# Performance work log

Measured on AMD Instinct MI355X. Metric: run time of the kernel, lower is better.

## Reference

```python
import jax, jax.numpy as jnp
import numpy as np

B, S, D_MODEL, D_KEY = 4, 2048, 1024, 128


def setup_inputs() -> dict:
    key = jax.random.key(0)
    kq, kk, kv, kwq, kwk, kwv = jax.random.split(key, 6)
    queries = jax.random.normal(kq, (B, S, D_MODEL), dtype=jnp.float32)
    keys = jax.random.normal(kk, (B, S, D_MODEL), dtype=jnp.float32)
    values = jax.random.normal(kv, (B, S, D_MODEL), dtype=jnp.float32)
    # causal mask: 1 where attention is allowed (j <= i), 0 otherwise
    mask = jnp.broadcast_to(jnp.tril(jnp.ones((S, S), dtype=jnp.int32)), (B, S, S))
    # torch nn.Linear weights are [out, in]; init ~ U(-1/sqrt(in), 1/sqrt(in))
    bound = 1.0 / np.sqrt(D_MODEL)
    Wq = jax.random.uniform(kwq, (D_KEY, D_MODEL), jnp.float32, -bound, bound)
    Wk = jax.random.uniform(kwk, (D_KEY, D_MODEL), jnp.float32, -bound, bound)
    Wv = jax.random.uniform(kwv, (D_KEY, D_MODEL), jnp.float32, -bound, bound)
    return {"queries": queries, "keys": keys, "values": values, "mask": mask,
            "Wq": Wq, "Wk": Wk, "Wv": Wv}


def reference(queries, keys, values, mask, Wq, Wk, Wv):
    d_key = Wq.shape[0]
    q = jnp.einsum('bsd,kd->bsk', queries, Wq)   # [B,S,d_key]
    k = jnp.einsum('bsd,kd->bsk', keys, Wk)
    v = jnp.einsum('bsd,kd->bsk', values, Wv)
    attn = jnp.einsum('bqk,bsk->bqs', q, k) / jnp.sqrt(jnp.float32(d_key))  # [B,S,S]
    attn = jnp.where(mask == 0, -jnp.inf, attn)
    attn = jax.nn.softmax(attn, axis=-1)
    return jnp.einsum('bqs,bsk->bqk', attn, v)   # [B,S,d_key]
```

## Files before the change

kernel.cpp:

```cpp
#include <hip/hip_runtime.h>
#include <hip/hip_bf16.h>

#define NB 4
#define SEQ 2048
#define DMODEL 1024
#define DKEY 128

using f32x4  = __attribute__((ext_vector_type(4))) float;
using bf16x8 = __attribute__((ext_vector_type(8))) short;
using u16x4  = __attribute__((ext_vector_type(4))) unsigned short;
using u16x8  = __attribute__((ext_vector_type(8))) unsigned short;

__device__ __forceinline__ unsigned short f2bf(float f) {
  __hip_bfloat16 h = __float2bfloat16(f);
  return __builtin_bit_cast(unsigned short, h);
}
__device__ __forceinline__ void gload16(const void* g, void* l) {
  __builtin_amdgcn_global_load_lds(
      (const __attribute__((address_space(1))) void*)g,
      (__attribute__((address_space(3))) void*)l, 16, 0, 0);
}

__global__ __launch_bounds__(256) void wconv_kernel(
    const float* __restrict__ Wq, const float* __restrict__ Wk,
    const float* __restrict__ Wv, unsigned short* __restrict__ Wb)
{
  int id = blockIdx.x * 256 + threadIdx.x;
  const float* src = (id < 16384) ? Wq : (id < 32768) ? Wk : Wv;
  int off = (id & 16383) * 8;
  float4 a = *reinterpret_cast<const float4*>(&src[off]);
  float4 b = *reinterpret_cast<const float4*>(&src[off + 4]);
  u16x8 p = { f2bf(a.x), f2bf(a.y), f2bf(a.z), f2bf(a.w),
              f2bf(b.x), f2bf(b.y), f2bf(b.z), f2bf(b.w) };
  *reinterpret_cast<u16x8*>(&Wb[(size_t)(id >> 14) * 131072 + off]) = p;
}

__global__ __launch_bounds__(256, 2) void proj_kernel(
    const float* __restrict__ Xq, const float* __restrict__ Xk, const float* __restrict__ Xv,
    const unsigned short* __restrict__ Wb,
    unsigned short* __restrict__ Yq, unsigned short* __restrict__ Yk,
    unsigned short* __restrict__ Vt)
{
  const int z = blockIdx.z;
  const float* X = (z == 0) ? Xq : (z == 1) ? Xk : Xv;
  const unsigned short* W = Wb + (size_t)z * 131072;

  __shared__ alignas(16) unsigned short XL[64 * 512];
  __shared__ alignas(16) unsigned short WL[2][128 * 32];

  const int t     = threadIdx.x;
  const int lane  = t & 63;
  const int w     = t >> 6;
  const int lr    = lane & 15;
  const int hi    = lane >> 4;
  const int rbase = hi * 4;
  const long m0   = (long)blockIdx.x * 64;
  const int arow  = w * 16 + lr;

  const int wg_row[2] = { (0 * 256 + t) >> 2, (1 * 256 + t) >> 2 };
  const int wg_col[2] = { ((((0 * 256 + t) & 3) ^ (wg_row[0] & 3)) << 3),
                          ((((1 * 256 + t) & 3) ^ (wg_row[1] & 3)) << 3) };

#define W_ISSUE(ks) do {                                                      \
    const int _s = (ks) & 1;                                                  \
    _Pragma("unroll")                                                         \
    for (int i = 0; i < 2; ++i)                                               \
      gload16(&W[(size_t)wg_row[i] * DMODEL + (ks) * 32 + wg_col[i]],         \
              &WL[_s][(i * 256 + w * 64) * 8]);                               \
  } while (0)

#define P1_LOAD(cbase) do {                                                   \
    for (int jb = 0; jb < 8; ++jb) {                                          \
      float4 v[4];                                                            \
      _Pragma("unroll")                                                       \
      for (int u = 0; u < 4; ++u) {                                           \
        int f = (jb * 4 + u) * 256 + t;                                       \
        int row = f >> 7, c4 = (f & 127) << 2;                                \
        v[u] = *reinterpret_cast<const float4*>(                              \
            &X[(m0 + row) * (long)DMODEL + (cbase) + c4]);                    \
      }                                                                       \
      _Pragma("unroll")                                                       \
      for (int u = 0; u < 4; ++u) {                                           \
        int f = (jb * 4 + u) * 256 + t;                                       \
        int row = f >> 7, c4 = (f & 127) << 2;                                \
        u16x4 p = { f2bf(v[u].x), f2bf(v[u].y), f2bf(v[u].z), f2bf(v[u].w) }; \
        *reinterpret_cast<u16x4*>(                                            \
            &XL[row * 512 + (((c4 >> 3) ^ (row & 7)) << 3)                    \
                + ((c4 >> 2) & 1) * 4]) = p;                                  \
      }                                                                       \
    }                                                                         \
  } while (0)

#define PJ_STEP(gks) do {                                                     \
    if ((gks) < 31) asm volatile("s_waitcnt vmcnt(2)" ::: "memory");          \
    else            asm volatile("s_waitcnt vmcnt(0)" ::: "memory");          \
    __builtin_amdgcn_s_barrier();                                             \
    {                                                                         \
      const int _s  = (gks) & 1;                                              \
      const int _gr = ((gks) & 15) * 4 + hi;                                  \
      bf16x8 a = *reinterpret_cast<const bf16x8*>(                            \
          &XL[arow * 512 + ((_gr ^ (lr & 7)) << 3)]);                         \
      _Pragma("unroll")                                                       \
      for (int n = 0; n < 8; ++n) {                                           \
        const int wrow = n * 16 + lr;                                         \
        bf16x8 b = *reinterpret_cast<const bf16x8*>(                          \
            &WL[_s][wrow * 32 + ((hi ^ (wrow & 3)) << 3)]);                   \
        acc[n] = __builtin_amdgcn_mfma_f32_16x16x32_bf16(a, b, acc[n], 0, 0, 0); \
      }                                                                       \
    }                                                                         \
    __builtin_amdgcn_s_barrier();                                             \
    if ((gks) + 2 < 32) W_ISSUE((gks) + 2);                                   \
  } while (0)

  f32x4 acc[8];
  const f32x4 zero = {0.f, 0.f, 0.f, 0.f};
#pragma unroll
  for (int n = 0; n < 8; ++n) acc[n] = zero;

  P1_LOAD(0);
  __syncthreads();
  W_ISSUE(0);
  W_ISSUE(1);
  for (int ks = 0; ks < 16; ++ks) PJ_STEP(ks);

  P1_LOAD(512);
  __syncthreads();
  for (int ks = 16; ks < 32; ++ks) PJ_STEP(ks);

#undef W_ISSUE
#undef P1_LOAD
#undef PJ_STEP

  if (z != 2) {
    unsigned short* Y = (z == 0) ? Yq : Yk;
#pragma unroll
    for (int n = 0; n < 8; ++n)
#pragma unroll
      for (int r = 0; r < 4; ++r) {
        long row = m0 + w * 16 + rbase + r;
        Y[row * DKEY + n * 16 + lr] = f2bf(acc[n][r]);
      }
  } else {
    unsigned short* Tl = XL;
    __syncthreads();
#pragma unroll
    for (int n = 0; n < 8; ++n)
#pragma unroll
      for (int r = 0; r < 4; ++r)
        Tl[(n * 16 + lr) * 72 + (w * 16 + rbase + r)] = f2bf(acc[n][r]);
    __syncthreads();
    const int bb = (int)(m0 >> 11);
    const int s0 = (int)(m0 & 2047);
#pragma unroll
    for (int i = 0; i < 4; ++i) {
      int id = t + 256 * i;
      int dr = id >> 3;
      int c8 = (id & 7) << 3;
      u16x8 v = *reinterpret_cast<const u16x8*>(&Tl[dr * 72 + c8]);
      *reinterpret_cast<u16x8*>(&Vt[((size_t)bb * DKEY + dr) * SEQ + s0 + c8]) = v;
    }
  }
}

__global__ __launch_bounds__(512, 2) void attn_kernel(
    const unsigned short* __restrict__ Q,
    const unsigned short* __restrict__ K,
    const unsigned short* __restrict__ Vt,
    float* __restrict__ O)
{
  const int  L    = blockIdx.x;
  const int  b    = (L & 7) >> 1;
  const int  qt   = 63 - (((L >> 3) << 1) | (L & 1));
  const int  q0   = qt * 32;
  const long base = (long)b * SEQ;
  const int  nt   = (q0 >> 6) + 1;
  const int  nsteps = (nt + 3) >> 2;

  __shared__ alignas(16) unsigned short Kl[4][64][128];
  __shared__ alignas(16) unsigned short Vl[4][128][64];
  __shared__ alignas(16) unsigned short Plds[8][16][72];
  __shared__ float Sm[4][32], Sl[4][32];

  const int t     = threadIdx.x;
  const int lane  = t & 63;
  const int w     = t >> 6;
  const int g     = w >> 1;
  const int wq    = w & 1;
  const int lr    = lane & 15;
  const int hi    = lane >> 4;
  const int lk    = hi * 8;
  const int rbase = hi * 4;

  bf16x8 qa[4];
  {
    const long qrow = (base + q0 + wq * 16 + lr) * (long)DKEY;
#pragma unroll
    for (int dk = 0; dk < 4; ++dk)
      qa[dk] = *reinterpret_cast<const bf16x8*>(&Q[qrow + dk * 32 + lk]);
  }

  const f32x4 zero = {0.f, 0.f, 0.f, 0.f};
  f32x4 oacc[8];
#pragma unroll
  for (int n = 0; n < 8; ++n) oacc[n] = zero;
  float m_run[4], l_run[4];
#pragma unroll
  for (int r = 0; r < 4; ++r) { m_run[r] = -1e30f; l_run[r] = 0.0f; }

  const float sc = 0.08838834764831845f;
  const unsigned short* VtB = Vt + (size_t)b * DKEY * SEQ;

  for (int st = 0; st < nsteps; ++st) {
    const int kt  = st * 4 + g;
    const bool act = kt < nt;
    const int kv0 = kt * 64;

    if (act) {
      const unsigned short* Kp = K + (base + kv0) * (long)DKEY;
#pragma unroll
      for (int it = 0; it < 8; ++it) {
        int c = it * 128 + wq * 64 + lane;
        int row = c >> 4, sl = (c & 15) ^ (row & 7);
        *reinterpret_cast<u16x8*>(&Kl[g][row][sl * 8]) =
            *reinterpret_cast<const u16x8*>(&Kp[(size_t)c * 8]);
      }
#pragma unroll
      for (int it = 0; it < 8; ++it) {
        int c = it * 128 + wq * 64 + lane;
        int d = c >> 3, sl = c & 7, slp = sl ^ (d & 7);
        *reinterpret_cast<u16x8*>(&Vl[g][d][slp * 8]) =
            *reinterpret_cast<const u16x8*>(&VtB[(size_t)d * SEQ + kv0 + sl * 8]);
      }
    }
    __syncthreads();

    if (act) {
      f32x4 s[4];
#pragma unroll
      for (int kc = 0; kc < 4; ++kc) {
        s[kc] = zero;
#pragma unroll
        for (int dk = 0; dk < 4; ++dk) {
          bf16x8 kb = *reinterpret_cast<const bf16x8*>(
              &Kl[g][kc * 16 + lr][((dk * 4 + hi) ^ (lr & 7)) * 8]);
          s[kc] = __builtin_amdgcn_mfma_f32_16x16x32_bf16(qa[dk], kb, s[kc], 0, 0, 0);
        }
      }

      const bool dmask = (kt == nt - 1);
      float x[4][4];
#pragma unroll
      for (int kc = 0; kc < 4; ++kc)
#pragma unroll
        for (int r = 0; r < 4; ++r) {
          float xv = s[kc][r] * sc;
          if (dmask) {
            int col  = kv0 + kc * 16 + lr;
            int rowq = q0 + wq * 16 + rbase + r;
            if (col > rowq) xv = -1e30f;
          }
          x[kc][r] = xv;
        }

#pragma unroll
      for (int r = 0; r < 4; ++r) {
        float tm = fmaxf(fmaxf(x[0][r], x[1][r]), fmaxf(x[2][r], x[3][r]));
        tm = fmaxf(tm, __shfl_xor(tm, 1));
        tm = fmaxf(tm, __shfl_xor(tm, 2));
        tm = fmaxf(tm, __shfl_xor(tm, 4));
        tm = fmaxf(tm, __shfl_xor(tm, 8));
        float mnew = fmaxf(m_run[r], tm);
        float scl  = __expf(m_run[r] - mnew);
        m_run[r] = mnew;
        float ps = 0.0f;
#pragma unroll
        for (int kc = 0; kc < 4; ++kc) {
          float pp = __expf(x[kc][r] - mnew);
          ps += pp;
          Plds[w][rbase + r][kc * 16 + lr] = f2bf(pp);
        }
        ps += __shfl_xor(ps, 1);
        ps += __shfl_xor(ps, 2);
        ps += __shfl_xor(ps, 4);
        ps += __shfl_xor(ps, 8);
        l_run[r] = l_run[r] * scl + ps;
#pragma unroll
        for (int n = 0; n < 8; ++n) oacc[n][r] *= scl;
      }

#pragma unroll
      for (int kk = 0; kk < 2; ++kk) {
        bf16x8 pa = *reinterpret_cast<const bf16x8*>(&Plds[w][lr][kk * 32 + lk]);
#pragma unroll
        for (int n = 0; n < 8; ++n) {
          bf16x8 vb = *reinterpret_cast<const bf16x8*>(
              &Vl[g][n * 16 + lr][((kk * 4 + hi) ^ (lr & 7)) * 8]);
          oacc[n] = __builtin_amdgcn_mfma_f32_16x16x32_bf16(pa, vb, oacc[n], 0, 0, 0);
        }
      }
    }
    __syncthreads();
  }

  float* Om = reinterpret_cast<float*>(&Kl[0][0][0]);
#pragma unroll
  for (int n = 0; n < 8; ++n)
#pragma unroll
    for (int r = 0; r < 4; ++r)
      Om[(g * 32 + wq * 16 + rbase + r) * 128 + n * 16 + lr] = oacc[n][r];
  if (lr == 0) {
#pragma unroll
    for (int r = 0; r < 4; ++r) {
      Sm[g][wq * 16 + rbase + r] = m_run[r];
      Sl[g][wq * 16 + rbase + r] = l_run[r];
    }
  }
  __syncthreads();

  const int row = t >> 4;
  const int c0  = (t & 15) * 8;
  float mM = fmaxf(fmaxf(Sm[0][row], Sm[1][row]), fmaxf(Sm[2][row], Sm[3][row]));
  float wts[4], lsum = 0.0f;
#pragma unroll
  for (int gv = 0; gv < 4; ++gv) {
    wts[gv] = __expf(Sm[gv][row] - mM);
    lsum += wts[gv] * Sl[gv][row];
  }
  const float linv = 1.0f / lsum;
  f32x4 o0 = zero, o1 = zero;
#pragma unroll
  for (int gv = 0; gv < 4; ++gv) {
    const float* src = &Om[(gv * 32 + row) * 128 + c0];
    f32x4 a0 = *reinterpret_cast<const f32x4*>(src);
    f32x4 a1 = *reinterpret_cast<const f32x4*>(src + 4);
    const float wt = wts[gv];
#pragma unroll
    for (int j = 0; j < 4; ++j) { o0[j] += wt * a0[j]; o1[j] += wt * a1[j]; }
  }
#pragma unroll
  for (int j = 0; j < 4; ++j) { o0[j] *= linv; o1[j] *= linv; }
  float* op = &O[(base + q0 + row) * (long)DKEY + c0];
  *reinterpret_cast<f32x4*>(op)     = o0;
  *reinterpret_cast<f32x4*>(op + 4) = o1;
}

extern "C" void kernel_launch(void* const* d_in, const int* in_sizes, int n_in,
                              void* d_out, int out_size, void* d_ws, size_t ws_size,
                              hipStream_t stream) {
  const float* Xq = (const float*)d_in[0];
  const float* Xk = (const float*)d_in[1];
  const float* Xv = (const float*)d_in[2];
  const float* Wq = (const float*)d_in[4];
  const float* Wk = (const float*)d_in[5];
  const float* Wv = (const float*)d_in[6];

  unsigned short* qp  = (unsigned short*)d_ws;
  unsigned short* kp  = qp + (size_t)NB * SEQ * DKEY;
  unsigned short* vtp = kp + (size_t)NB * SEQ * DKEY;
  unsigned short* wbp = (unsigned short*)d_out;

  hipLaunchKernelGGL(wconv_kernel, dim3(192), dim3(256), 0, stream,
                     Wq, Wk, Wv, wbp);
  dim3 g1(SEQ * NB / 64, 1, 3);
  hipLaunchKernelGGL(proj_kernel, g1, dim3(256), 0, stream,
                     Xq, Xk, Xv, wbp, qp, kp, vtp);
  hipLaunchKernelGGL(attn_kernel, dim3(256), dim3(512), 0, stream,
                     qp, kp, vtp, (float*)d_out);
}
```

Before: 70.76 us.

## Fuse weight conversion, projections and attention into one persistent kernel with flags

Merges the three launches into one kernel of 256 blocks. Each block first projects its Q, K or V tiles, converting fp32 weights to bf16 on the fly in LDS instead of in a separate pass, then sets a completion flag. The block then spin-waits on the flags for the K/V tiles it needs before running causal attention. This removes two kernel launches and the weight conversion pass, and lets projection overlap with attention. In exchange it relies on all 256 blocks being co-resident so the spin-waits cannot deadlock, adds a memset and atomics, and halves projection occupancy per block.

Result: slower. 135.6 us (+91.7%).

```diff
diff --git a/kernel.cpp b/kernel.cpp
--- a/kernel.cpp
+++ b/kernel.cpp
@@ -15,78 +15,74 @@
   __hip_bfloat16 h = __float2bfloat16(f);
   return __builtin_bit_cast(unsigned short, h);
 }
+__device__ __forceinline__ bf16x8 pack8(f32x4 lo, f32x4 hi) {
+  u16x8 p = { f2bf(lo[0]), f2bf(lo[1]), f2bf(lo[2]), f2bf(lo[3]),
+              f2bf(hi[0]), f2bf(hi[1]), f2bf(hi[2]), f2bf(hi[3]) };
+  return __builtin_bit_cast(bf16x8, p);
+}
 __device__ __forceinline__ void gload16(const void* g, void* l) {
   __builtin_amdgcn_global_load_lds(
       (const __attribute__((address_space(1))) void*)g,
       (__attribute__((address_space(3))) void*)l, 16, 0, 0);
 }
-
-__global__ __launch_bounds__(256) void wconv_kernel(
-    const float* __restrict__ Wq, const float* __restrict__ Wk,
-    const float* __restrict__ Wv, unsigned short* __restrict__ Wb)
+__device__ __forceinline__ void spinflag(int* f) {
+  while (atomicAdd(f, 0) == 0) __builtin_amdgcn_s_sleep(8);
+}
+
+#define SMEM_BYTES 150528
+
+__device__ __forceinline__ void proj_unit(
+    const float* __restrict__ X, const float* __restrict__ W,
+    unsigned short* Y, unsigned short* VtB_or_null,
+    int u, char* SMEM, int t, int* flags, int fidx)
 {
-  int id = blockIdx.x * 256 + threadIdx.x;
-  const float* src = (id < 16384) ? Wq : (id < 32768) ? Wk : Wv;
-  int off = (id & 16383) * 8;
-  float4 a = *reinterpret_cast<const float4*>(&src[off]);
-  float4 b = *reinterpret_cast<const float4*>(&src[off + 4]);
-  u16x8 p = { f2bf(a.x), f2bf(a.y), f2bf(a.z), f2bf(a.w),
-              f2bf(b.x), f2bf(b.y), f2bf(b.z), f2bf(b.w) };
-  *reinterpret_cast<u16x8*>(&Wb[(size_t)(id >> 14) * 131072 + off]) = p;
-}
-
-__global__ __launch_bounds__(256, 2) void proj_kernel(
-    const float* __restrict__ Xq, const float* __restrict__ Xk, const float* __restrict__ Xv,
-    const unsigned short* __restrict__ Wb,
-    unsigned short* __restrict__ Yq, unsigned short* __restrict__ Yk,
-    unsigned short* __restrict__ Vt)
-{
-  const int z = blockIdx.z;
-  const float* X = (z == 0) ? Xq : (z == 1) ? Xk : Xv;
-  const unsigned short* W = Wb + (size_t)z * 131072;
-
-  __shared__ alignas(16) unsigned short XL[64 * 512];
-  __shared__ alignas(16) unsigned short WL[2][128 * 32];
-
-  const int t     = threadIdx.x;
+  unsigned short* XL = reinterpret_cast<unsigned short*>(SMEM);
+  float*          WL = reinterpret_cast<float*>(SMEM + 65536);
+
   const int lane  = t & 63;
   const int w     = t >> 6;
+  const int wm    = w >> 1;
+  const int wn    = w & 1;
   const int lr    = lane & 15;
   const int hi    = lane >> 4;
   const int rbase = hi * 4;
-  const long m0   = (long)blockIdx.x * 64;
-  const int arow  = w * 16 + lr;
-
-  const int wg_row[2] = { (0 * 256 + t) >> 2, (1 * 256 + t) >> 2 };
-  const int wg_col[2] = { ((((0 * 256 + t) & 3) ^ (wg_row[0] & 3)) << 3),
-                          ((((1 * 256 + t) & 3) ^ (wg_row[1] & 3)) << 3) };
+  const long m0   = (long)u * 64;
+  const int arow  = wm * 16 + lr;
+
+  int wrow_[2], wcol_[2];
+#pragma unroll
+  for (int i = 0; i < 2; ++i) {
+    int G = i * 512 + t;
+    wrow_[i] = G >> 3;
+    wcol_[i] = (((G & 7) ^ (wrow_[i] & 7)) << 2);
+  }
 
 #define W_ISSUE(ks) do {                                                      \
-    const int _s = (ks) & 1;                                                  \
+    float* _dst = WL + ((ks) & 1) * 4096;                                     \
     _Pragma("unroll")                                                         \
     for (int i = 0; i < 2; ++i)                                               \
-      gload16(&W[(size_t)wg_row[i] * DMODEL + (ks) * 32 + wg_col[i]],         \
-              &WL[_s][(i * 256 + w * 64) * 8]);                               \
+      gload16(&W[(size_t)wrow_[i] * DMODEL + (ks) * 32 + wcol_[i]],           \
+              _dst + (i * 512 + w * 64) * 4);                                 \
   } while (0)
 
 #define P1_LOAD(cbase) do {                                                   \
-    for (int jb = 0; jb < 8; ++jb) {                                          \
+    for (int jb = 0; jb < 4; ++jb) {                                          \
       float4 v[4];                                                            \
       _Pragma("unroll")                                                       \
-      for (int u = 0; u < 4; ++u) {                                           \
-        int f = (jb * 4 + u) * 256 + t;                                       \
+      for (int u4 = 0; u4 < 4; ++u4) {                                        \
+        int f = (jb * 4 + u4) * 512 + t;                                      \
         int row = f >> 7, c4 = (f & 127) << 2;                                \
-        v[u] = *reinterpret_cast<const float4*>(                              \
+        v[u4] = *reinterpret_cast<const float4*>(                             \
             &X[(m0 + row) * (long)DMODEL + (cbase) + c4]);                    \
       }                                                                       \
       _Pragma("unroll")                                                       \
-      for (int u = 0; u < 4; ++u) {                                           \
-        int f = (jb * 4 + u) * 256 + t;                                       \
+      for (int u4 = 0; u4 < 4; ++u4) {                                        \
+        int f = (jb * 4 + u4) * 512 + t;                                      \
         int row = f >> 7, c4 = (f & 127) << 2;                                \
-        u16x4 p = { f2bf(v[u].x), f2bf(v[u].y), f2bf(v[u].z), f2bf(v[u].w) }; \
+        u16x4 p = { f2bf(v[u4].x), f2bf(v[u4].y), f2bf(v[u4].z), f2bf(v[u4].w) }; \
         *reinterpret_cast<u16x4*>(                                            \
-            &XL[row * 512 + (((c4 >> 3) ^ (row & 7)) << 3)                    \
-                + ((c4 >> 2) & 1) * 4]) = p;                                  \
+            &XL[row * 512 + ((((c4 >> 3) ^ (row & 7)) << 3)                   \
+                + ((c4 >> 2) & 1) * 4)]) = p;                                 \
       }                                                                       \
     }                                                                         \
   } while (0)
@@ -96,33 +92,36 @@
     else            asm volatile("s_waitcnt vmcnt(0)" ::: "memory");          \
     __builtin_amdgcn_s_barrier();                                             \
     {                                                                         \
-      const int _s  = (gks) & 1;                                              \
+      const float* wbase = WL + ((gks) & 1) * 4096;                           \
       const int _gr = ((gks) & 15) * 4 + hi;                                  \
       bf16x8 a = *reinterpret_cast<const bf16x8*>(                            \
           &XL[arow * 512 + ((_gr ^ (lr & 7)) << 3)]);                         \
       _Pragma("unroll")                                                       \
-      for (int n = 0; n < 8; ++n) {                                           \
-        const int wrow = n * 16 + lr;                                         \
-        bf16x8 b = *reinterpret_cast<const bf16x8*>(                          \
-            &WL[_s][wrow * 32 + ((hi ^ (wrow & 3)) << 3)]);                   \
-        acc[n] = __builtin_amdgcn_mfma_f32_16x16x32_bf16(a, b, acc[n], 0, 0, 0); \
+      for (int n = 0; n < 4; ++n) {                                           \
+        const int wrow = wn * 64 + n * 16 + lr;                               \
+        f32x4 blo = *reinterpret_cast<const f32x4*>(                          \
+            &wbase[wrow * 32 + ((((hi * 2)     ^ (wrow & 7))) << 2)]);        \
+        f32x4 bhi = *reinterpret_cast<const f32x4*>(                          \
+            &wbase[wrow * 32 + ((((hi * 2 + 1) ^ (wrow & 7))) << 2)]);        \
+        acc[n] = __builtin_amdgcn_mfma_f32_16x16x32_bf16(a, pack8(blo, bhi),  \
+                                                         acc[n], 0, 0, 0);    \
       }                                                                       \
     }                                                                         \
     __builtin_amdgcn_s_barrier();                                             \
     if ((gks) + 2 < 32) W_ISSUE((gks) + 2);                                   \
   } while (0)
 
-  f32x4 acc[8];
+  f32x4 acc[4];
   const f32x4 zero = {0.f, 0.f, 0.f, 0.f};
 #pragma unroll
-  for (int n = 0; n < 8; ++n) acc[n] = zero;
-
+  for (int n = 0; n < 4; ++n) acc[n] = zero;
+
+  __syncthreads();
   P1_LOAD(0);
   __syncthreads();
   W_ISSUE(0);
   W_ISSUE(1);
   for (int ks = 0; ks < 16; ++ks) PJ_STEP(ks);
-
   P1_LOAD(512);
   __syncthreads();
   for (int ks = 16; ks < 32; ++ks) PJ_STEP(ks);
@@ -131,57 +130,83 @@
 #undef P1_LOAD
 #undef PJ_STEP
 
-  if (z != 2) {
-    unsigned short* Y = (z == 0) ? Yq : Yk;
-#pragma unroll
-    for (int n = 0; n < 8; ++n)
+  if (Y != nullptr) {
+#pragma unroll
+    for (int n = 0; n < 4; ++n)
 #pragma unroll
       for (int r = 0; r < 4; ++r) {
-        long row = m0 + w * 16 + rbase + r;
-        Y[row * DKEY + n * 16 + lr] = f2bf(acc[n][r]);
+        long row = m0 + wm * 16 + rbase + r;
+        Y[row * DKEY + wn * 64 + n * 16 + lr] = f2bf(acc[n][r]);
       }
   } else {
-    unsigned short* Tl = XL;
+    unsigned short* Tl = reinterpret_cast<unsigned short*>(SMEM);
     __syncthreads();
 #pragma unroll
-    for (int n = 0; n < 8; ++n)
+    for (int n = 0; n < 4; ++n)
 #pragma unroll
       for (int r = 0; r < 4; ++r)
-        Tl[(n * 16 + lr) * 72 + (w * 16 + rbase + r)] = f2bf(acc[n][r]);
+        Tl[(wn * 64 + n * 16 + lr) * 72 + (wm * 16 + rbase + r)] = f2bf(acc[n][r]);
     __syncthreads();
-    const int bb = (int)(m0 >> 11);
-    const int s0 = (int)(m0 & 2047);
-#pragma unroll
-    for (int i = 0; i < 4; ++i) {
-      int id = t + 256 * i;
+    const int bb = u >> 5;
+    const int s0 = (u & 31) * 64;
+    unsigned short* VtB = VtB_or_null + (size_t)bb * DKEY * SEQ;
+#pragma unroll
+    for (int i = 0; i < 2; ++i) {
+      int id = t + 512 * i;
       int dr = id >> 3;
       int c8 = (id & 7) << 3;
       u16x8 v = *reinterpret_cast<const u16x8*>(&Tl[dr * 72 + c8]);
-      *reinterpret_cast<u16x8*>(&Vt[((size_t)bb * DKEY + dr) * SEQ + s0 + c8]) = v;
+      *reinterpret_cast<u16x8*>(&VtB[(size_t)dr * SEQ + s0 + c8]) = v;
     }
   }
-}
-
-__global__ __launch_bounds__(512, 2) void attn_kernel(
-    const unsigned short* __restrict__ Q,
-    const unsigned short* __restrict__ K,
-    const unsigned short* __restrict__ Vt,
-    float* __restrict__ O)
+
+  __syncthreads();
+  if (t == 0) {
+    __threadfence();
+    atomicExch(&flags[fidx], 1);
+  }
+}
+
+__global__ __launch_bounds__(512, 1) void fused_kernel(
+    const float* __restrict__ Xq, const float* __restrict__ Xk, const float* __restrict__ Xv,
+    const float* __restrict__ Wq, const float* __restrict__ Wk, const float* __restrict__ Wv,
+    unsigned short* Qb, unsigned short* Kb, unsigned short* Vt,
+    int* flags, float* O)
 {
-  const int  L    = blockIdx.x;
-  const int  b    = (L & 7) >> 1;
-  const int  qt   = 63 - (((L >> 3) << 1) | (L & 1));
+  __shared__ __align__(16) char SMEM[SMEM_BYTES];
+  const int B = blockIdx.x;
+  const int t = threadIdx.x;
+
+  if (B < 128) {
+    proj_unit(Xk, Wk, Kb, nullptr, B, SMEM, t, flags, B);
+    proj_unit(Xv, Wv, nullptr, Vt, B, SMEM, t, flags, 128 + B);
+  } else {
+    proj_unit(Xq, Wq, Qb, nullptr, B - 128, SMEM, t, flags, 256 + (B - 128));
+  }
+
+  int b, qt;
+  if (B < 128) { b = B >> 5; qt = B & 31; }
+  else         { int i = B - 128; b = i >> 5; qt = 32 + (i & 31); }
+
+  const int jmax = qt >> 1;
+  if (t <= jmax)                         spinflag(&flags[b * 32 + t]);
+  else if (t >= 64 && t < 64 + jmax + 1) spinflag(&flags[128 + b * 32 + (t - 64)]);
+  else if (t == 160)                     spinflag(&flags[256 + b * 32 + jmax]);
+  __syncthreads();
+  __threadfence();
+
+  typedef unsigned short us;
+  us (*Kl)[64][128]  = reinterpret_cast<us(*)[64][128]>(SMEM);
+  us (*Vl)[128][64]  = reinterpret_cast<us(*)[128][64]>(SMEM + 65536);
+  us (*Plds)[16][72] = reinterpret_cast<us(*)[16][72]>(SMEM + 131072);
+  float (*Sm)[32]    = reinterpret_cast<float(*)[32]>(SMEM + 149504);
+  float (*Sl)[32]    = reinterpret_cast<float(*)[32]>(SMEM + 150016);
+
   const int  q0   = qt * 32;
   const long base = (long)b * SEQ;
   const int  nt   = (q0 >> 6) + 1;
   const int  nsteps = (nt + 3) >> 2;
 
-  __shared__ alignas(16) unsigned short Kl[4][64][128];
-  __shared__ alignas(16) unsigned short Vl[4][128][64];
-  __shared__ alignas(16) unsigned short Plds[8][16][72];
-  __shared__ float Sm[4][32], Sl[4][32];
-
-  const int t     = threadIdx.x;
   const int lane  = t & 63;
   const int w     = t >> 6;
   const int g     = w >> 1;
@@ -196,7 +221,7 @@
     const long qrow = (base + q0 + wq * 16 + lr) * (long)DKEY;
 #pragma unroll
     for (int dk = 0; dk < 4; ++dk)
-      qa[dk] = *reinterpret_cast<const bf16x8*>(&Q[qrow + dk * 32 + lk]);
+      qa[dk] = *reinterpret_cast<const bf16x8*>(&Qb[qrow + dk * 32 + lk]);
   }
 
   const f32x4 zero = {0.f, 0.f, 0.f, 0.f};
@@ -216,7 +241,7 @@
     const int kv0 = kt * 64;
 
     if (act) {
-      const unsigned short* Kp = K + (base + kv0) * (long)DKEY;
+      const unsigned short* Kp = Kb + (base + kv0) * (long)DKEY;
 #pragma unroll
       for (int it = 0; it < 8; ++it) {
         int c = it * 128 + wq * 64 + lane;
@@ -302,7 +327,7 @@
     __syncthreads();
   }
 
-  float* Om = reinterpret_cast<float*>(&Kl[0][0][0]);
+  float* Om = reinterpret_cast<float*>(SMEM);
 #pragma unroll
   for (int n = 0; n < 8; ++n)
 #pragma unroll
@@ -357,13 +382,9 @@
   unsigned short* qp  = (unsigned short*)d_ws;
   unsigned short* kp  = qp + (size_t)NB * SEQ * DKEY;
   unsigned short* vtp = kp + (size_t)NB * SEQ * DKEY;
-  unsigned short* wbp = (unsigned short*)d_out;
-
-  hipLaunchKernelGGL(wconv_kernel, dim3(192), dim3(256), 0, stream,
-                     Wq, Wk, Wv, wbp);
-  dim3 g1(SEQ * NB / 64, 1, 3);
-  hipLaunchKernelGGL(proj_kernel, g1, dim3(256), 0, stream,
-                     Xq, Xk, Xv, wbp, qp, kp, vtp);
-  hipLaunchKernelGGL(attn_kernel, dim3(256), dim3(512), 0, stream,
-                     qp, kp, vtp, (float*)d_out);
-}
+  int* flags = (int*)((char*)d_ws + ((size_t)6 << 20));
+
+  hipMemsetAsync(flags, 0, 4096, stream);
+  hipLaunchKernelGGL(fused_kernel, dim3(256), dim3(512), 0, stream,
+                     Xq, Xk, Xv, Wq, Wk, Wv, qp, kp, vtp, flags, (float*)d_out);
+}
```
